# Optimization experiments

Hardware: AMD Instinct MI355X
Metric: run time of the kernel (lower is better)

## Reference

```python
import jax, jax.numpy as jnp
import numpy as np

N = 1_000_000   # gaussians
K_NB = 10       # neighbor control points per gaussian
K_TOTAL = 300   # num_fine control points


def _normalize(q, eps=1e-8):
    return q / jnp.maximum(jnp.linalg.norm(q, axis=-1, keepdims=True), eps)


def quaternion_to_rotation_matrix(q):
    # q: [..., 4] in (w, x, y, z); normalized before conversion
    q = _normalize(q)
    w, x, y, z = q[..., 0], q[..., 1], q[..., 2], q[..., 3]
    R = jnp.stack([
        jnp.stack([1 - 2 * (y * y + z * z), 2 * (x * y - w * z), 2 * (x * z + w * y)], axis=-1),
        jnp.stack([2 * (x * y + w * z), 1 - 2 * (x * x + z * z), 2 * (y * z - w * x)], axis=-1),
        jnp.stack([2 * (x * z - w * y), 2 * (y * z + w * x), 1 - 2 * (x * x + y * y)], axis=-1),
    ], axis=-2)  # [..., 3, 3]
    return R


def quaternion_multiply(a, b):
    # Hamilton product, (w, x, y, z)
    aw, ax, ay, az = a[..., 0], a[..., 1], a[..., 2], a[..., 3]
    bw, bx, by, bz = b[..., 0], b[..., 1], b[..., 2], b[..., 3]
    return jnp.stack([
        aw * bw - ax * bx - ay * by - az * bz,
        aw * bx + ax * bw + ay * bz - az * by,
        aw * by - ax * bz + ay * bw + az * bx,
        aw * bz + ax * by - ay * bx + az * bw,
    ], axis=-1)


def setup_inputs() -> dict:
    key = jax.random.key(0)
    ks = jax.random.split(key, 7)
    means = jax.random.normal(ks[0], (N, 3), dtype=jnp.float32)
    quaternions = _normalize(jax.random.normal(ks[1], (N, 4), dtype=jnp.float32))
    w = jax.random.uniform(ks[2], (N, K_NB), dtype=jnp.float32) + 1e-3
    weights = w / w.sum(-1, keepdims=True)  # blending weights sum to 1
    indices = jax.random.randint(ks[3], (N, K_NB), 0, K_TOTAL)
    ctrl_translations = 0.1 * jax.random.normal(ks[4], (K_TOTAL, 3), dtype=jnp.float32)
    ctrl_rotations = _normalize(jax.random.normal(ks[5], (K_TOTAL, 4), dtype=jnp.float32))
    ctrl_positions = jax.random.normal(ks[6], (K_TOTAL, 3), dtype=jnp.float32)
    return {
        'means': means, 'quaternions': quaternions, 'weights': weights,
        'ctrl_translations': ctrl_translations, 'ctrl_rotations': ctrl_rotations,
        'ctrl_positions': ctrl_positions, 'indices': indices,
    }


def reference(means, quaternions, weights, ctrl_translations, ctrl_rotations, ctrl_positions, indices):
    # gather neighbor control-point transforms
    nb_trans = ctrl_translations[indices]   # [N, K, 3]
    nb_rots = ctrl_rotations[indices]       # [N, K, 4]
    nb_pos = ctrl_positions[indices]        # [N, K, 3]

    diff = means[:, None, :] - nb_pos                       # [N, K, 3]
    R_ctrl = quaternion_to_rotation_matrix(nb_rots)         # [N, K, 3, 3]
    rotated_diff = jnp.einsum('nkij,nkj->nki', R_ctrl, diff)
    deformed_per_cp = rotated_diff + nb_pos + nb_trans      # [N, K, 3]

    w = weights[..., None]                                  # [N, K, 1]
    deformed_means = (w * deformed_per_cp).sum(axis=1)      # [N, 3]

    blended_rot = _normalize((w * nb_rots).sum(axis=1))     # [N, 4]
    deformed_quats = quaternion_multiply(blended_rot, quaternions)
    return deformed_means, deformed_quats
```

## Files before the change

kernel.cpp:

```cpp
#include <hip/hip_runtime.h>
#include <math.h>


__device__ __forceinline__ void compute_cp(
    const float* __restrict__ ctrl_trans,
    const float* __restrict__ ctrl_rot,
    const float* __restrict__ ctrl_pos,
    int cp, float4* q_out, float4* b_out)
{
    float4 qv = ((const float4*)ctrl_rot)[cp];
    float qw = qv.x, qx = qv.y, qy = qv.z, qz = qv.w;
    float n   = sqrtf(qw * qw + qx * qx + qy * qy + qz * qz);
    float inv = 1.0f / fmaxf(n, 1e-8f);
    float w = qw * inv, x = qx * inv, y = qy * inv, z = qz * inv;
    float R00 = 1.0f - 2.0f * (y * y + z * z);
    float R01 = 2.0f * (x * y - w * z);
    float R02 = 2.0f * (x * z + w * y);
    float R10 = 2.0f * (x * y + w * z);
    float R11 = 1.0f - 2.0f * (x * x + z * z);
    float R12 = 2.0f * (y * z - w * x);
    float R20 = 2.0f * (x * z - w * y);
    float R21 = 2.0f * (y * z + w * x);
    float R22 = 1.0f - 2.0f * (x * x + y * y);
    float px = ctrl_pos[cp * 3 + 0];
    float py = ctrl_pos[cp * 3 + 1];
    float pz = ctrl_pos[cp * 3 + 2];
    float tx = ctrl_trans[cp * 3 + 0];
    float ty = ctrl_trans[cp * 3 + 1];
    float tz = ctrl_trans[cp * 3 + 2];
    *q_out = make_float4(w, x, y, z);
    *b_out = make_float4(px + tx - (R00 * px + R01 * py + R02 * pz),
                         py + ty - (R10 * px + R11 * py + R12 * pz),
                         pz + tz - (R20 * px + R21 * py + R22 * pz),
                         0.0f);
}

struct Accum {
    float W;
    float Mxx, Myy, Mzz, Mxy, Mxz, Myz, Mwx, Mwy, Mwz;
    float qsw, qsx, qsy, qsz;
    float bsx, bsy, bsz;
};

__device__ __forceinline__ void acc_init(Accum& a) {
    a.W = 0.0f;
    a.Mxx = a.Myy = a.Mzz = 0.0f;
    a.Mxy = a.Mxz = a.Myz = 0.0f;
    a.Mwx = a.Mwy = a.Mwz = 0.0f;
    a.qsw = a.qsx = a.qsy = a.qsz = 0.0f;
    a.bsx = a.bsy = a.bsz = 0.0f;
}

__device__ __forceinline__ void acc_neighbor(Accum& a, const float4* __restrict__ s4,
                                             int K_TOTAL, int cp, float w) {
    float4 q = s4[cp];
    float4 b = s4[K_TOTAL + cp];
    float tw = w * q.x, tx = w * q.y, ty = w * q.z, tz = w * q.w;
    a.W += w;
    a.Mxx = fmaf(tx, q.y, a.Mxx);
    a.Myy = fmaf(ty, q.z, a.Myy);
    a.Mzz = fmaf(tz, q.w, a.Mzz);
    a.Mxy = fmaf(tx, q.z, a.Mxy);
    a.Mxz = fmaf(tx, q.w, a.Mxz);
    a.Myz = fmaf(ty, q.w, a.Myz);
    a.Mwx = fmaf(tw, q.y, a.Mwx);
    a.Mwy = fmaf(tw, q.z, a.Mwy);
    a.Mwz = fmaf(tw, q.w, a.Mwz);
    a.qsw += tw; a.qsx += tx; a.qsy += ty; a.qsz += tz;
    a.bsx = fmaf(w, b.x, a.bsx);
    a.bsy = fmaf(w, b.y, a.bsy);
    a.bsz = fmaf(w, b.z, a.bsz);
}

__device__ __forceinline__ void acc_epilogue(const Accum& a,
                                             float mx, float my, float mz,
                                             float4 g,
                                             float* dmx, float* dmy, float* dmz,
                                             float4* oq) {
    float A00 = a.W - 2.0f * (a.Myy + a.Mzz);
    float A01 = 2.0f * (a.Mxy - a.Mwz);
    float A02 = 2.0f * (a.Mxz + a.Mwy);
    float A10 = 2.0f * (a.Mxy + a.Mwz);
    float A11 = a.W - 2.0f * (a.Mxx + a.Mzz);
    float A12 = 2.0f * (a.Myz - a.Mwx);
    float A20 = 2.0f * (a.Mxz - a.Mwy);
    float A21 = 2.0f * (a.Myz + a.Mwx);
    float A22 = a.W - 2.0f * (a.Mxx + a.Myy);

    *dmx = fmaf(A00, mx, fmaf(A01, my, fmaf(A02, mz, a.bsx)));
    *dmy = fmaf(A10, mx, fmaf(A11, my, fmaf(A12, mz, a.bsy)));
    *dmz = fmaf(A20, mx, fmaf(A21, my, fmaf(A22, mz, a.bsz)));

    float n   = sqrtf(a.qsw * a.qsw + a.qsx * a.qsx + a.qsy * a.qsy + a.qsz * a.qsz);
    float inv = 1.0f / fmaxf(n, 1e-8f);
    float bw = a.qsw * inv, bx = a.qsx * inv, by = a.qsy * inv, bz = a.qsz * inv;

    float gw = g.x, gx = g.y, gy = g.z, gz = g.w;
    oq->x = bw * gw - bx * gx - by * gy - bz * gz;
    oq->y = bw * gx + bx * gw + by * gz - bz * gy;
    oq->z = bw * gy - bx * gz + by * gw + bz * gx;
    oq->w = bw * gz + bx * gy - by * gx + bz * gw;
}

__global__ __launch_bounds__(256) void deform_pair_kernel(
    const float* __restrict__ means,
    const float* __restrict__ quats,
    const float* __restrict__ weights,
    const float* __restrict__ ctrl_trans,
    const float* __restrict__ ctrl_rot,
    const float* __restrict__ ctrl_pos,
    const int*   __restrict__ indices,
    float* __restrict__ out_means,
    float* __restrict__ out_quats,
    int N, int K_TOTAL, long long n_pairs)
{
    extern __shared__ float4 s4[];
    for (int cp = threadIdx.x; cp < K_TOTAL; cp += blockDim.x) {
        float4 q, b;
        compute_cp(ctrl_trans, ctrl_rot, ctrl_pos, cp, &q, &b);
        s4[cp]           = q;
        s4[K_TOTAL + cp] = b;
    }
    __syncthreads();

    long long stride = (long long)gridDim.x * blockDim.x;
    for (long long p = (long long)blockIdx.x * blockDim.x + threadIdx.x;
         p < n_pairs; p += stride) {
        long long i0 = 2 * p;

        if (i0 + 1 < N) {
            const int4*   ip = (const int4*)(indices + i0 * 10);
            const float4* wp = (const float4*)(weights + i0 * 10);
            int4   I0 = ip[0], I1 = ip[1], I2 = ip[2], I3 = ip[3], I4 = ip[4];
            float4 W0 = wp[0], W1 = wp[1], W2 = wp[2], W3 = wp[3], W4 = wp[4];
            const float2* mp = (const float2*)(means + i0 * 3);
            float2 m01 = mp[0], m23 = mp[1], m45 = mp[2];
            float4 g0 = ((const float4*)quats)[i0];
            float4 g1 = ((const float4*)quats)[i0 + 1];

            Accum a0; acc_init(a0);
            acc_neighbor(a0, s4, K_TOTAL, I0.x, W0.x);
            acc_neighbor(a0, s4, K_TOTAL, I0.y, W0.y);
            acc_neighbor(a0, s4, K_TOTAL, I0.z, W0.z);
            acc_neighbor(a0, s4, K_TOTAL, I0.w, W0.w);
            acc_neighbor(a0, s4, K_TOTAL, I1.x, W1.x);
            acc_neighbor(a0, s4, K_TOTAL, I1.y, W1.y);
            acc_neighbor(a0, s4, K_TOTAL, I1.z, W1.z);
            acc_neighbor(a0, s4, K_TOTAL, I1.w, W1.w);
            acc_neighbor(a0, s4, K_TOTAL, I2.x, W2.x);
            acc_neighbor(a0, s4, K_TOTAL, I2.y, W2.y);

            Accum a1; acc_init(a1);
            acc_neighbor(a1, s4, K_TOTAL, I2.z, W2.z);
            acc_neighbor(a1, s4, K_TOTAL, I2.w, W2.w);
            acc_neighbor(a1, s4, K_TOTAL, I3.x, W3.x);
            acc_neighbor(a1, s4, K_TOTAL, I3.y, W3.y);
            acc_neighbor(a1, s4, K_TOTAL, I3.z, W3.z);
            acc_neighbor(a1, s4, K_TOTAL, I3.w, W3.w);
            acc_neighbor(a1, s4, K_TOTAL, I4.x, W4.x);
            acc_neighbor(a1, s4, K_TOTAL, I4.y, W4.y);
            acc_neighbor(a1, s4, K_TOTAL, I4.z, W4.z);
            acc_neighbor(a1, s4, K_TOTAL, I4.w, W4.w);

            float d0x, d0y, d0z, d1x, d1y, d1z;
            float4 oq0, oq1;
            acc_epilogue(a0, m01.x, m01.y, m23.x, g0, &d0x, &d0y, &d0z, &oq0);
            acc_epilogue(a1, m23.y, m45.x, m45.y, g1, &d1x, &d1y, &d1z, &oq1);

            float2* omp = (float2*)(out_means + i0 * 3);
            omp[0] = make_float2(d0x, d0y);
            omp[1] = make_float2(d0z, d1x);
            omp[2] = make_float2(d1y, d1z);

            float4* oqp = (float4*)(out_quats + i0 * 4);
            oqp[0] = oq0;
            oqp[1] = oq1;
        } else {
            const int*   idx_row = indices + i0 * 10;
            const float* w_row   = weights + i0 * 10;
            Accum a0; acc_init(a0);
#pragma unroll
            for (int k = 0; k < 10; k++)
                acc_neighbor(a0, s4, K_TOTAL, idx_row[k], w_row[k]);

            float mx = means[i0 * 3 + 0];
            float my = means[i0 * 3 + 1];
            float mz = means[i0 * 3 + 2];
            float4 g0 = ((const float4*)quats)[i0];
            float dx, dy, dz;
            float4 oq0;
            acc_epilogue(a0, mx, my, mz, g0, &dx, &dy, &dz, &oq0);
            out_means[i0 * 3 + 0] = dx;
            out_means[i0 * 3 + 1] = dy;
            out_means[i0 * 3 + 2] = dz;
            ((float4*)out_quats)[i0] = oq0;
        }
    }
}

__global__ __launch_bounds__(256) void deform_generic_kernel(
    const float* __restrict__ means,
    const float* __restrict__ quats,
    const float* __restrict__ weights,
    const float* __restrict__ ctrl_trans,
    const float* __restrict__ ctrl_rot,
    const float* __restrict__ ctrl_pos,
    const int*   __restrict__ indices,
    float* __restrict__ out_means,
    float* __restrict__ out_quats,
    int N, int K_NB, int K_TOTAL)
{
    extern __shared__ float4 s4[];
    for (int cp = threadIdx.x; cp < K_TOTAL; cp += blockDim.x) {
        float4 q, b;
        compute_cp(ctrl_trans, ctrl_rot, ctrl_pos, cp, &q, &b);
        s4[cp]           = q;
        s4[K_TOTAL + cp] = b;
    }
    __syncthreads();

    long long i = (long long)blockIdx.x * blockDim.x + threadIdx.x;
    if (i >= N) return;

    const int*   idx_row = indices + i * K_NB;
    const float* w_row   = weights + i * K_NB;
    Accum a0; acc_init(a0);
    for (int k = 0; k < K_NB; k++)
        acc_neighbor(a0, s4, K_TOTAL, idx_row[k], w_row[k]);

    float mx = means[i * 3 + 0];
    float my = means[i * 3 + 1];
    float mz = means[i * 3 + 2];
    float4 g0 = ((const float4*)quats)[i];
    float dx, dy, dz;
    float4 oq0;
    acc_epilogue(a0, mx, my, mz, g0, &dx, &dy, &dz, &oq0);
    out_means[i * 3 + 0] = dx;
    out_means[i * 3 + 1] = dy;
    out_means[i * 3 + 2] = dz;
    ((float4*)out_quats)[i] = oq0;
}

extern "C" void kernel_launch(void* const* d_in, const int* in_sizes, int n_in,
                              void* d_out, int out_size, void* d_ws, size_t ws_size,
                              hipStream_t stream) {
    const float* means      = (const float*)d_in[0];
    const float* quats      = (const float*)d_in[1];
    const float* weights    = (const float*)d_in[2];
    const float* ctrl_trans = (const float*)d_in[3];
    const float* ctrl_rot   = (const float*)d_in[4];
    const float* ctrl_pos   = (const float*)d_in[5];
    const int*   indices    = (const int*)d_in[6];

    int N       = in_sizes[0] / 3;
    int K_NB    = in_sizes[2] / N;
    int K_TOTAL = in_sizes[3] / 3;

    float* out_means = (float*)d_out;
    float* out_quats = (float*)d_out + (long long)N * 3;

    int block = 256;
    size_t smem = (size_t)K_TOTAL * 2 * sizeof(float4);

    if (K_NB == 10) {
        long long n_pairs = ((long long)N + 1) / 2;
        long long blocks  = (n_pairs + block - 1) / block;
        int grid = (int)(blocks < 1536 ? blocks : 1536);
        deform_pair_kernel<<<grid, block, smem, stream>>>(
            means, quats, weights, ctrl_trans, ctrl_rot, ctrl_pos, indices,
            out_means, out_quats, N, K_TOTAL, n_pairs);
    } else {
        int grid = (int)(((long long)N + block - 1) / block);
        deform_generic_kernel<<<grid, block, smem, stream>>>(
            means, quats, weights, ctrl_trans, ctrl_rot, ctrl_pos, indices,
            out_means, out_quats, N, K_NB, K_TOTAL);
    }
}
```

Measured before the change: 152.2 us.

## Stage indices and weights through LDS with coalesced loads, one gaussian per thread

Replaces the persistent pair-per-thread kernel with a non-persistent kernel where each 256-thread block first copies its 2560 indices and weights into shared memory using coalesced float4 loads, then each thread reads its row from LDS. The goal is fully coalesced global reads for the per-gaussian neighbor data instead of strided 40-byte-per-thread vector loads. In exchange every block now rebuilds the 300-entry control-point table (about 4k blocks instead of 1536), uses more LDS per block, and gives up the two-gaussian register pairing.

```diff
diff --git a/kernel.cpp b/kernel.cpp
--- a/kernel.cpp
+++ b/kernel.cpp
@@ -1,39 +1,6 @@
 #include <hip/hip_runtime.h>
 #include <math.h>
 
-
-__device__ __forceinline__ void compute_cp(
-    const float* __restrict__ ctrl_trans,
-    const float* __restrict__ ctrl_rot,
-    const float* __restrict__ ctrl_pos,
-    int cp, float4* q_out, float4* b_out)
-{
-    float4 qv = ((const float4*)ctrl_rot)[cp];
-    float qw = qv.x, qx = qv.y, qy = qv.z, qz = qv.w;
-    float n   = sqrtf(qw * qw + qx * qx + qy * qy + qz * qz);
-    float inv = 1.0f / fmaxf(n, 1e-8f);
-    float w = qw * inv, x = qx * inv, y = qy * inv, z = qz * inv;
-    float R00 = 1.0f - 2.0f * (y * y + z * z);
-    float R01 = 2.0f * (x * y - w * z);
-    float R02 = 2.0f * (x * z + w * y);
-    float R10 = 2.0f * (x * y + w * z);
-    float R11 = 1.0f - 2.0f * (x * x + z * z);
-    float R12 = 2.0f * (y * z - w * x);
-    float R20 = 2.0f * (x * z - w * y);
-    float R21 = 2.0f * (y * z + w * x);
-    float R22 = 1.0f - 2.0f * (x * x + y * y);
-    float px = ctrl_pos[cp * 3 + 0];
-    float py = ctrl_pos[cp * 3 + 1];
-    float pz = ctrl_pos[cp * 3 + 2];
-    float tx = ctrl_trans[cp * 3 + 0];
-    float ty = ctrl_trans[cp * 3 + 1];
-    float tz = ctrl_trans[cp * 3 + 2];
-    *q_out = make_float4(w, x, y, z);
-    *b_out = make_float4(px + tx - (R00 * px + R01 * py + R02 * pz),
-                         py + ty - (R10 * px + R11 * py + R12 * pz),
-                         pz + tz - (R20 * px + R21 * py + R22 * pz),
-                         0.0f);
-}
 
 struct Accum {
     float W;
@@ -51,10 +18,10 @@
     a.bsx = a.bsy = a.bsz = 0.0f;
 }
 
-__device__ __forceinline__ void acc_neighbor(Accum& a, const float4* __restrict__ s4,
+__device__ __forceinline__ void acc_neighbor(Accum& a, const float4* __restrict__ tbl,
                                              int K_TOTAL, int cp, float w) {
-    float4 q = s4[cp];
-    float4 b = s4[K_TOTAL + cp];
+    float4 q = tbl[cp];
+    float4 b = tbl[K_TOTAL + cp];
     float tw = w * q.x, tx = w * q.y, ty = w * q.z, tz = w * q.w;
     a.W += w;
     a.Mxx = fmaf(tx, q.y, a.Mxx);
@@ -102,7 +69,42 @@
     oq->w = bw * gz + bx * gy - by * gx + bz * gw;
 }
 
-__global__ __launch_bounds__(256) void deform_pair_kernel(
+__device__ __forceinline__ void build_table(
+    const float* __restrict__ ctrl_trans,
+    const float* __restrict__ ctrl_rot,
+    const float* __restrict__ ctrl_pos,
+    float4* __restrict__ tbl, int K_TOTAL)
+{
+    for (int cp = threadIdx.x; cp < K_TOTAL; cp += blockDim.x) {
+        float4 qv = ((const float4*)ctrl_rot)[cp];
+        float qw = qv.x, qx = qv.y, qy = qv.z, qz = qv.w;
+        float nn  = sqrtf(qw * qw + qx * qx + qy * qy + qz * qz);
+        float inv = 1.0f / fmaxf(nn, 1e-8f);
+        float w = qw * inv, x = qx * inv, y = qy * inv, z = qz * inv;
+        float R00 = 1.0f - 2.0f * (y * y + z * z);
+        float R01 = 2.0f * (x * y - w * z);
+        float R02 = 2.0f * (x * z + w * y);
+        float R10 = 2.0f * (x * y + w * z);
+        float R11 = 1.0f - 2.0f * (x * x + z * z);
+        float R12 = 2.0f * (y * z - w * x);
+        float R20 = 2.0f * (x * z - w * y);
+        float R21 = 2.0f * (y * z + w * x);
+        float R22 = 1.0f - 2.0f * (x * x + y * y);
+        float px = ctrl_pos[cp * 3 + 0];
+        float py = ctrl_pos[cp * 3 + 1];
+        float pz = ctrl_pos[cp * 3 + 2];
+        float tx = ctrl_trans[cp * 3 + 0];
+        float ty = ctrl_trans[cp * 3 + 1];
+        float tz = ctrl_trans[cp * 3 + 2];
+        tbl[cp]           = make_float4(w, x, y, z);
+        tbl[K_TOTAL + cp] = make_float4(px + tx - (R00 * px + R01 * py + R02 * pz),
+                                        py + ty - (R10 * px + R11 * py + R12 * pz),
+                                        pz + tz - (R20 * px + R21 * py + R22 * pz),
+                                        0.0f);
+    }
+}
+
+__global__ __launch_bounds__(256) void deform_stage_kernel(
     const float* __restrict__ means,
     const float* __restrict__ quats,
     const float* __restrict__ weights,
@@ -112,90 +114,78 @@
     const int*   __restrict__ indices,
     float* __restrict__ out_means,
     float* __restrict__ out_quats,
-    int N, int K_TOTAL, long long n_pairs)
+    int N, int K_TOTAL)
 {
-    extern __shared__ float4 s4[];
-    for (int cp = threadIdx.x; cp < K_TOTAL; cp += blockDim.x) {
-        float4 q, b;
-        compute_cp(ctrl_trans, ctrl_rot, ctrl_pos, cp, &q, &b);
-        s4[cp]           = q;
-        s4[K_TOTAL + cp] = b;
+    extern __shared__ float smem[];
+    float4* tbl  = (float4*)smem;
+    float*  sIdx = smem + 8 * K_TOTAL;
+    float*  sW   = sIdx + 2560;
+
+    const int t = threadIdx.x;
+    const long long blockBase = (long long)blockIdx.x * 256;
+    const long long fbase = blockBase * 10;
+    const long long ftot  = (long long)N * 10;
+
+#pragma unroll
+    for (int j = t; j < 640; j += 256) {
+        long long f0 = fbase + 4LL * j;
+        float4 vi, vw;
+        if (f0 + 3 < ftot) {
+            vi = ((const float4*)indices)[f0 / 4];
+            vw = ((const float4*)weights)[f0 / 4];
+        } else {
+            float ei[4], ew[4];
+#pragma unroll
+            for (int e = 0; e < 4; e++) {
+                long long f = f0 + e;
+                bool ok = f < ftot;
+                ei[e] = ok ? ((const float*)indices)[f] : 0.0f;
+                ew[e] = ok ? weights[f] : 0.0f;
+            }
+            vi = make_float4(ei[0], ei[1], ei[2], ei[3]);
+            vw = make_float4(ew[0], ew[1], ew[2], ew[3]);
+        }
+        *(float4*)(sIdx + 4 * j) = vi;
+        *(float4*)(sW   + 4 * j) = vw;
     }
+
+    build_table(ctrl_trans, ctrl_rot, ctrl_pos, tbl, K_TOTAL);
+
     __syncthreads();
 
-    long long stride = (long long)gridDim.x * blockDim.x;
-    for (long long p = (long long)blockIdx.x * blockDim.x + threadIdx.x;
-         p < n_pairs; p += stride) {
-        long long i0 = 2 * p;
-
-        if (i0 + 1 < N) {
-            const int4*   ip = (const int4*)(indices + i0 * 10);
-            const float4* wp = (const float4*)(weights + i0 * 10);
-            int4   I0 = ip[0], I1 = ip[1], I2 = ip[2], I3 = ip[3], I4 = ip[4];
-            float4 W0 = wp[0], W1 = wp[1], W2 = wp[2], W3 = wp[3], W4 = wp[4];
-            const float2* mp = (const float2*)(means + i0 * 3);
-            float2 m01 = mp[0], m23 = mp[1], m45 = mp[2];
-            float4 g0 = ((const float4*)quats)[i0];
-            float4 g1 = ((const float4*)quats)[i0 + 1];
-
-            Accum a0; acc_init(a0);
-            acc_neighbor(a0, s4, K_TOTAL, I0.x, W0.x);
-            acc_neighbor(a0, s4, K_TOTAL, I0.y, W0.y);
-            acc_neighbor(a0, s4, K_TOTAL, I0.z, W0.z);
-            acc_neighbor(a0, s4, K_TOTAL, I0.w, W0.w);
-            acc_neighbor(a0, s4, K_TOTAL, I1.x, W1.x);
-            acc_neighbor(a0, s4, K_TOTAL, I1.y, W1.y);
-            acc_neighbor(a0, s4, K_TOTAL, I1.z, W1.z);
-            acc_neighbor(a0, s4, K_TOTAL, I1.w, W1.w);
-            acc_neighbor(a0, s4, K_TOTAL, I2.x, W2.x);
-            acc_neighbor(a0, s4, K_TOTAL, I2.y, W2.y);
-
-            Accum a1; acc_init(a1);
-            acc_neighbor(a1, s4, K_TOTAL, I2.z, W2.z);
-            acc_neighbor(a1, s4, K_TOTAL, I2.w, W2.w);
-            acc_neighbor(a1, s4, K_TOTAL, I3.x, W3.x);
-            acc_neighbor(a1, s4, K_TOTAL, I3.y, W3.y);
-            acc_neighbor(a1, s4, K_TOTAL, I3.z, W3.z);
-            acc_neighbor(a1, s4, K_TOTAL, I3.w, W3.w);
-            acc_neighbor(a1, s4, K_TOTAL, I4.x, W4.x);
-            acc_neighbor(a1, s4, K_TOTAL, I4.y, W4.y);
-            acc_neighbor(a1, s4, K_TOTAL, I4.z, W4.z);
-            acc_neighbor(a1, s4, K_TOTAL, I4.w, W4.w);
-
-            float d0x, d0y, d0z, d1x, d1y, d1z;
-            float4 oq0, oq1;
-            acc_epilogue(a0, m01.x, m01.y, m23.x, g0, &d0x, &d0y, &d0z, &oq0);
-            acc_epilogue(a1, m23.y, m45.x, m45.y, g1, &d1x, &d1y, &d1z, &oq1);
-
-            float2* omp = (float2*)(out_means + i0 * 3);
-            omp[0] = make_float2(d0x, d0y);
-            omp[1] = make_float2(d0z, d1x);
-            omp[2] = make_float2(d1y, d1z);
-
-            float4* oqp = (float4*)(out_quats + i0 * 4);
-            oqp[0] = oq0;
-            oqp[1] = oq1;
-        } else {
-            const int*   idx_row = indices + i0 * 10;
-            const float* w_row   = weights + i0 * 10;
-            Accum a0; acc_init(a0);
-#pragma unroll
-            for (int k = 0; k < 10; k++)
-                acc_neighbor(a0, s4, K_TOTAL, idx_row[k], w_row[k]);
-
-            float mx = means[i0 * 3 + 0];
-            float my = means[i0 * 3 + 1];
-            float mz = means[i0 * 3 + 2];
-            float4 g0 = ((const float4*)quats)[i0];
-            float dx, dy, dz;
-            float4 oq0;
-            acc_epilogue(a0, mx, my, mz, g0, &dx, &dy, &dz, &oq0);
-            out_means[i0 * 3 + 0] = dx;
-            out_means[i0 * 3 + 1] = dy;
-            out_means[i0 * 3 + 2] = dz;
-            ((float4*)out_quats)[i0] = oq0;
-        }
-    }
+    long long g = blockBase + t;
+    if (g >= N) return;
+
+    const int2*   ip2 = (const int2*)  (sIdx + t * 10);
+    const float2* wp2 = (const float2*)(sW   + t * 10);
+    int2   i01 = ip2[0], i23 = ip2[1], i45 = ip2[2], i67 = ip2[3], i89 = ip2[4];
+    float2 w01 = wp2[0], w23 = wp2[1], w45 = wp2[2], w67 = wp2[3], w89 = wp2[4];
+
+    float mx = means[g * 3 + 0];
+    float my = means[g * 3 + 1];
+    float mz = means[g * 3 + 2];
+    float4 gq = ((const float4*)quats)[g];
+
+    Accum a; acc_init(a);
+    acc_neighbor(a, tbl, K_TOTAL, i01.x, w01.x);
+    acc_neighbor(a, tbl, K_TOTAL, i01.y, w01.y);
+    acc_neighbor(a, tbl, K_TOTAL, i23.x, w23.x);
+    acc_neighbor(a, tbl, K_TOTAL, i23.y, w23.y);
+    acc_neighbor(a, tbl, K_TOTAL, i45.x, w45.x);
+    acc_neighbor(a, tbl, K_TOTAL, i45.y, w45.y);
+    acc_neighbor(a, tbl, K_TOTAL, i67.x, w67.x);
+    acc_neighbor(a, tbl, K_TOTAL, i67.y, w67.y);
+    acc_neighbor(a, tbl, K_TOTAL, i89.x, w89.x);
+    acc_neighbor(a, tbl, K_TOTAL, i89.y, w89.y);
+
+    float dx, dy, dz;
+    float4 oq;
+    acc_epilogue(a, mx, my, mz, gq, &dx, &dy, &dz, &oq);
+
+    out_means[g * 3 + 0] = dx;
+    out_means[g * 3 + 1] = dy;
+    out_means[g * 3 + 2] = dz;
+    ((float4*)out_quats)[g] = oq;
 }
 
 __global__ __launch_bounds__(256) void deform_generic_kernel(
@@ -210,13 +200,9 @@
     float* __restrict__ out_quats,
     int N, int K_NB, int K_TOTAL)
 {
-    extern __shared__ float4 s4[];
-    for (int cp = threadIdx.x; cp < K_TOTAL; cp += blockDim.x) {
-        float4 q, b;
-        compute_cp(ctrl_trans, ctrl_rot, ctrl_pos, cp, &q, &b);
-        s4[cp]           = q;
-        s4[K_TOTAL + cp] = b;
-    }
+    extern __shared__ float smem[];
+    float4* tbl = (float4*)smem;
+    build_table(ctrl_trans, ctrl_rot, ctrl_pos, tbl, K_TOTAL);
     __syncthreads();
 
     long long i = (long long)blockIdx.x * blockDim.x + threadIdx.x;
@@ -224,21 +210,21 @@
 
     const int*   idx_row = indices + i * K_NB;
     const float* w_row   = weights + i * K_NB;
-    Accum a0; acc_init(a0);
+    Accum a; acc_init(a);
     for (int k = 0; k < K_NB; k++)
-        acc_neighbor(a0, s4, K_TOTAL, idx_row[k], w_row[k]);
+        acc_neighbor(a, tbl, K_TOTAL, idx_row[k], w_row[k]);
 
     float mx = means[i * 3 + 0];
     float my = means[i * 3 + 1];
     float mz = means[i * 3 + 2];
-    float4 g0 = ((const float4*)quats)[i];
+    float4 gq = ((const float4*)quats)[i];
     float dx, dy, dz;
-    float4 oq0;
-    acc_epilogue(a0, mx, my, mz, g0, &dx, &dy, &dz, &oq0);
+    float4 oq;
+    acc_epilogue(a, mx, my, mz, gq, &dx, &dy, &dz, &oq);
     out_means[i * 3 + 0] = dx;
     out_means[i * 3 + 1] = dy;
     out_means[i * 3 + 2] = dz;
-    ((float4*)out_quats)[i] = oq0;
+    ((float4*)out_quats)[i] = oq;
 }
 
 extern "C" void kernel_launch(void* const* d_in, const int* in_sizes, int n_in,
@@ -260,17 +246,15 @@
     float* out_quats = (float*)d_out + (long long)N * 3;
 
     int block = 256;
-    size_t smem = (size_t)K_TOTAL * 2 * sizeof(float4);
+    int grid  = (int)(((long long)N + block - 1) / block);
 
     if (K_NB == 10) {
-        long long n_pairs = ((long long)N + 1) / 2;
-        long long blocks  = (n_pairs + block - 1) / block;
-        int grid = (int)(blocks < 1536 ? blocks : 1536);
-        deform_pair_kernel<<<grid, block, smem, stream>>>(
+        size_t smem = (size_t)(8 * K_TOTAL + 5120) * sizeof(float);
+        deform_stage_kernel<<<grid, block, smem, stream>>>(
             means, quats, weights, ctrl_trans, ctrl_rot, ctrl_pos, indices,
-            out_means, out_quats, N, K_TOTAL, n_pairs);
+            out_means, out_quats, N, K_TOTAL);
     } else {
-        int grid = (int)(((long long)N + block - 1) / block);
+        size_t smem = (size_t)K_TOTAL * 2 * sizeof(float4);
         deform_generic_kernel<<<grid, block, smem, stream>>>(
             means, quats, weights, ctrl_trans, ctrl_rot, ctrl_pos, indices,
             out_means, out_quats, N, K_NB, K_TOTAL);
```

Result: faster. 148.8 us (-2.3%).
